# Kernel tuning notes

Hardware: AMD Instinct MI355X
Metric: run time of the kernel (lower is better)

The kernel has to match this reference:

```python
import jax, jax.numpy as jnp
import numpy as np

LEAK = 0.01  # torch LeakyReLU default negative_slope

def lrelu(x):
    return jnp.where(x >= 0, x, LEAK * x)

def edge_conv(x, src, dst, ea, W1, b1, W2, b2):
    # message: cat(x_i=target, x_j=source, edge_attr) -> Linear -> LeakyReLU -> Linear
    m = jnp.concatenate([x[dst], x[src], ea], axis=1)          # [E, 2F+Fe]
    h = lrelu(m @ W1 + b1) @ W2 + b2                            # [E, H]
    n = x.shape[0]
    agg = jnp.full((n, h.shape[1]), jnp.inf, h.dtype).at[dst].min(h)  # scatter-min at target
    return jnp.where(jnp.isfinite(agg), agg, jnp.zeros_like(agg))     # empty nodes -> 0


def setup_inputs() -> dict:
    key = jax.random.key(0)
    ks = jax.random.split(key, 20)
    B, N, E = 4, 20000, 640000
    NF, AD, EF, H = 2, 1, 1, 8
    inp = {
        "node_features": jax.random.randint(ks[0], (B, N, NF), 0, 10, dtype=jnp.int32),
        "actions": jax.random.normal(ks[1], (B, N), dtype=jnp.float32),
        "edge_index": jax.random.randint(ks[2], (B, 2, E), 0, N, dtype=jnp.int64),
        "edge_features": jax.random.normal(ks[3], (B, E, EF), dtype=jnp.float32),
    }
    d0 = NF + AD  # 3
    def lin(k, fin, fout):
        s = 1.0 / np.sqrt(fin)
        k1, k2 = jax.random.split(k)
        return (jax.random.uniform(k1, (fin, fout), jnp.float32, -s, s),
                jax.random.uniform(k2, (fout,), jnp.float32, -s, s))
    inp["c1_W1"], inp["c1_b1"] = lin(ks[4], 2 * d0 + EF, H)
    inp["c1_W2"], inp["c1_b2"] = lin(ks[5], H, H)
    inp["c2_W1"], inp["c2_b1"] = lin(ks[6], 2 * H + 1, H)
    inp["c2_W2"], inp["c2_b2"] = lin(ks[7], H, H)
    inp["c3_W1"], inp["c3_b1"] = lin(ks[8], 2 * H + 1, H)
    inp["c3_W2"], inp["c3_b2"] = lin(ks[9], H, H)
    inp["lin_W"], inp["lin_b"] = lin(ks[10], d0 + H, 1)
    return inp


def reference(node_features, actions, edge_index, edge_features,
              c1_W1, c1_b1, c1_W2, c1_b2,
              c2_W1, c2_b1, c2_W2, c2_b2,
              c3_W1, c3_b1, c3_W2, c3_b2,
              lin_W, lin_b):
    # x = int(node_features) concat actions  -> float
    x0 = jnp.concatenate([node_features.astype(jnp.int32).astype(jnp.float32),
                          actions[..., None]], axis=-1)  # [B,N,3]

    def per_graph(x0g, eig, eag):
        src, dst = eig[0], eig[1]  # flow source_to_target: x_j=src, x_i=dst
        h = lrelu(edge_conv(x0g, src, dst, eag, c1_W1, c1_b1, c1_W2, c1_b2))
        h = lrelu(edge_conv(h, src, dst, eag, c2_W1, c2_b1, c2_W2, c2_b2))
        h = lrelu(edge_conv(h, src, dst, eag, c3_W1, c3_b1, c3_W2, c3_b2))
        xc = jnp.concatenate([x0g, h], axis=1)  # [N, 3+8]
        return jnp.sum(xc, axis=0)              # sum-pool over nodes

    pooled = jax.vmap(per_graph)(x0, edge_index, edge_features)  # [B, 11]
    return pooled @ lin_W + lin_b  # [B, 1]
```

## Files before the change

kernel.cpp:

```cpp
#include <hip/hip_runtime.h>

#define LEAK 0.01f
#define BS 128
#define PCHUNK 4096
#define PT 256
#define CT 512
#define MAXNB 256
#define CPGMAX 256

__device__ __forceinline__ float lrelu(float v) {
    return v >= 0.f ? v : LEAK * v;
}

__device__ __forceinline__ unsigned int fmin_encode(float x) {
    unsigned int u = __float_as_uint(x);
    return (u & 0x80000000u) ? ~u : (u | 0x80000000u);
}
__device__ __forceinline__ float fmin_decode(unsigned int k) {
    unsigned int u = (k & 0x80000000u) ? (k ^ 0x80000000u) : ~k;
    return __uint_as_float(u);
}

__device__ __forceinline__ void block_add(float c, float* dst) {
    __shared__ float wsum[8];
#pragma unroll
    for (int off = 32; off > 0; off >>= 1) c += __shfl_down(c, off, 64);
    int lane = threadIdx.x & 63;
    int wave = threadIdx.x >> 6;
    if (lane == 0) wsum[wave] = c;
    __syncthreads();
    if (threadIdx.x == 0) {
        float s = 0.f;
        int nw = blockDim.x >> 6;
        for (int w = 0; w < nw; ++w) s += wsum[w];
        atomicAdd(dst, s);
    }
}

__global__ __launch_bounds__(256) void init_pre1_kernel(
    const int* __restrict__ nf, const float* __restrict__ act,
    const float* __restrict__ W1, const float* __restrict__ b1,
    const float* __restrict__ lw, const float* __restrict__ lb,
    float* __restrict__ a1, float* __restrict__ a2,
    float* __restrict__ out, int N) {
    int b = blockIdx.y;
    int n = blockIdx.x * 256 + threadIdx.x;
    float c = 0.f;
    if (n < N) {
        size_t i = (size_t)b * N + n;
        float x0 = (float)nf[i * 2 + 0];
        float x1 = (float)nf[i * 2 + 1];
        float x2 = act[i];
        float v1[8], v2[8];
#pragma unroll
        for (int j = 0; j < 8; ++j) {
            v1[j] = b1[j] + x0 * W1[0 * 8 + j] + x1 * W1[1 * 8 + j] + x2 * W1[2 * 8 + j];
            v2[j] =         x0 * W1[3 * 8 + j] + x1 * W1[4 * 8 + j] + x2 * W1[5 * 8 + j];
        }
        float4* o1 = (float4*)(a1 + i * 8);
        float4* o2 = (float4*)(a2 + i * 8);
        o1[0] = make_float4(v1[0], v1[1], v1[2], v1[3]);
        o1[1] = make_float4(v1[4], v1[5], v1[6], v1[7]);
        o2[0] = make_float4(v2[0], v2[1], v2[2], v2[3]);
        o2[1] = make_float4(v2[4], v2[5], v2[6], v2[7]);
        c = x0 * lw[0] + x1 * lw[1] + x2 * lw[2];
        if (n == 0) c += lb[0];
    }
    block_add(c, &out[b]);
}

__global__ __launch_bounds__(PT) void part_kernel(
    const int* __restrict__ ei, const float* __restrict__ ea,
    int2* __restrict__ pairs, int* __restrict__ ofs,
    int E, int NB, int CPG) {
    __shared__ int lc[MAXNB];
    __shared__ int lofs[MAXNB + 1];
    __shared__ int ts[PT];
    int b = blockIdx.y;
    int c = blockIdx.x;
    int t = threadIdx.x;
    for (int i = t; i < NB; i += PT) lc[i] = 0;
    __syncthreads();

    int e0 = c * PCHUNK;
    int end = min(e0 + PCHUNK, E);
    const int* srow = ei + (size_t)b * 2 * E;
    const int* drow = srow + E;

    int pk[PCHUNK / PT];
#pragma unroll
    for (int j = 0; j < PCHUNK / PT; ++j) {
        int e = e0 + j * PT + t;
        int p = -1;
        if (e < end) {
            int d = drow[e];
            int bin = d >> 7;
            int r = atomicAdd(&lc[bin], 1);
            p = bin | ((d & 127) << 10) | (r << 17);
        }
        pk[j] = p;
    }
    __syncthreads();

    int v = (t < NB) ? lc[t] : 0;
    ts[t] = v;
    __syncthreads();
    int incl = v;
    for (int off = 1; off < PT; off <<= 1) {
        int add = (t >= off) ? ts[t - off] : 0;
        __syncthreads();
        incl += add;
        ts[t] = incl;
        __syncthreads();
    }
    if (t < NB) lofs[t] = incl - v;
    if (t == PT - 1) lofs[NB] = incl;
    __syncthreads();

    int* og = ofs + ((size_t)b * CPG + c) * (NB + 1);
    for (int i = t; i <= NB; i += PT) {
        int w = lofs[i];
        og[i] = w;
        if (i < NB) lc[i] = w;
    }
    __syncthreads();

    size_t pbase = (size_t)b * E + e0;
#pragma unroll
    for (int j = 0; j < PCHUNK / PT; ++j) {
        int e = e0 + j * PT + t;
        if (e < end) {
            int p = pk[j];
            int bin = p & 1023;
            int dl = (p >> 10) & 127;
            int r = p >> 17;
            int pos = lc[bin] + r;
            pairs[pbase + pos] =
                make_int2(srow[e] | (dl << 16), __float_as_int(ea[(size_t)b * E + e]));
        }
    }
}


__device__ __forceinline__ void conv_edge_body(
    const float* __restrict__ a2g, const float* we, const float* bb,
    const float* __restrict__ W2, int2 p,
    const float* __restrict__ a1s, unsigned int* __restrict__ acc) {
    int srcn = p.x & 0xFFFF;
    int dl = (p.x >> 16) & 127;
    float eav = __int_as_float(p.y);
    const float4* q = (const float4*)(a2g + (size_t)srcn * 8);
    float4 lo = q[0], hi = q[1];
    float h1[8];
    h1[0] = a1s[dl * 9 + 0] + lo.x; h1[1] = a1s[dl * 9 + 1] + lo.y;
    h1[2] = a1s[dl * 9 + 2] + lo.z; h1[3] = a1s[dl * 9 + 3] + lo.w;
    h1[4] = a1s[dl * 9 + 4] + hi.x; h1[5] = a1s[dl * 9 + 5] + hi.y;
    h1[6] = a1s[dl * 9 + 6] + hi.z; h1[7] = a1s[dl * 9 + 7] + hi.w;
#pragma unroll
    for (int j = 0; j < 8; ++j) {
        h1[j] = fmaf(eav, we[j], h1[j]);
        h1[j] = lrelu(h1[j]);
    }
    float h2[8];
#pragma unroll
    for (int j = 0; j < 8; ++j) h2[j] = bb[j];
#pragma unroll
    for (int kk = 0; kk < 8; ++kk) {
        float hk = h1[kk];
#pragma unroll
        for (int j = 0; j < 8; ++j) h2[j] = fmaf(hk, W2[kk * 8 + j], h2[j]);
    }
#pragma unroll
    for (int j = 0; j < 8; ++j)
        atomicMin(&acc[dl * 9 + j], fmin_encode(h2[j]));
}

__device__ __forceinline__ void conv_edges_runs(
    const float* __restrict__ a2g, const float* we, const float* bb,
    const float* __restrict__ W2, const int2* __restrict__ pairsg,
    const int* __restrict__ ofsg, int bin, int NB, int CPG,
    const float* __restrict__ a1s, unsigned int* __restrict__ acc,
    int* __restrict__ rs, int* __restrict__ re) {
    int t = threadIdx.x;
    for (int c = t; c < CPG; c += CT) {
        const int* o = ofsg + (size_t)c * (NB + 1) + bin;
        rs[c] = o[0];
        re[c] = o[1];
    }
    __syncthreads();
    int sw = t >> 5;
    int sub = t & 31;
    const int nsw = CT >> 5;
    for (int c = sw; c < CPG; c += nsw) {
        int cb = c * PCHUNK;
        int k1 = cb + re[c];
        for (int k = cb + rs[c] + sub; k < k1; k += 32)
            conv_edge_body(a2g, we, bb, W2, pairsg[k], a1s, acc);
    }
}

__global__ __launch_bounds__(CT) void conv_mid_kernel(
    const float* __restrict__ a1, const float* __restrict__ a2,
    const float* __restrict__ w1e, const float* __restrict__ W2,
    const float* __restrict__ b2,
    const float* __restrict__ nW1, const float* __restrict__ nb1,
    const int* __restrict__ ofs, const int2* __restrict__ pairs,
    float* __restrict__ na1, float* __restrict__ na2,
    int N, int NB, int CPG, int E) {
    __shared__ float a1s[BS * 9];
    __shared__ unsigned int acc[BS * 9];
    __shared__ int rs[CPGMAX];
    __shared__ int re[CPGMAX];
    int b = blockIdx.y;
    int bin = blockIdx.x;
    int n0 = bin << 7;
    int nCnt = min(BS, N - n0);
    int t = threadIdx.x;
    size_t gn0 = ((size_t)b * N + n0) * 8;

    for (int i = t; i < nCnt * 8; i += CT)
        a1s[(i >> 3) * 9 + (i & 7)] = a1[gn0 + i];
    for (int i = t; i < BS * 9; i += CT) acc[i] = 0xFFFFFFFFu;
    float we[8], bb[8];
#pragma unroll
    for (int j = 0; j < 8; ++j) { we[j] = w1e[j]; bb[j] = b2[j]; }
    __syncthreads();

    conv_edges_runs(a2 + (size_t)b * N * 8, we, bb, W2,
                    pairs + (size_t)b * E, ofs + (size_t)b * CPG * (NB + 1),
                    bin, NB, CPG, a1s, acc, rs, re);
    __syncthreads();

    for (int i = t; i < nCnt * 8; i += CT) {
        float v = fmin_decode(acc[(i >> 3) * 9 + (i & 7)]);
        unsigned int u = __float_as_uint(v);
        if ((u & 0x7F800000u) == 0x7F800000u) v = 0.f;
        a1s[(i >> 3) * 9 + (i & 7)] = lrelu(v);
    }
    __syncthreads();

    int node = t >> 1, half = t & 1;
    if (node < nCnt) {
        float h[8];
#pragma unroll
        for (int j = 0; j < 8; ++j) h[j] = a1s[node * 9 + j];
        float v[8];
#pragma unroll
        for (int j = 0; j < 8; ++j) v[j] = half ? 0.f : nb1[j];
        const float* Wbase = nW1 + (half ? 64 : 0);
#pragma unroll
        for (int k = 0; k < 8; ++k) {
            float hk = h[k];
#pragma unroll
            for (int j = 0; j < 8; ++j) v[j] = fmaf(hk, Wbase[k * 8 + j], v[j]);
        }
        float* dst = (half ? na2 : na1) + gn0 + (size_t)node * 8;
        float4* o = (float4*)dst;
        o[0] = make_float4(v[0], v[1], v[2], v[3]);
        o[1] = make_float4(v[4], v[5], v[6], v[7]);
    }
}

__global__ __launch_bounds__(CT) void conv_final_kernel(
    const float* __restrict__ a1, const float* __restrict__ a2,
    const float* __restrict__ w1e, const float* __restrict__ W2,
    const float* __restrict__ b2, const float* __restrict__ lw,
    const int* __restrict__ ofs, const int2* __restrict__ pairs,
    float* __restrict__ out, int N, int NB, int CPG, int E) {
    __shared__ float a1s[BS * 9];
    __shared__ unsigned int acc[BS * 9];
    __shared__ int rs[CPGMAX];
    __shared__ int re[CPGMAX];
    int b = blockIdx.y;
    int bin = blockIdx.x;
    int n0 = bin << 7;
    int nCnt = min(BS, N - n0);
    int t = threadIdx.x;
    size_t gn0 = ((size_t)b * N + n0) * 8;

    for (int i = t; i < nCnt * 8; i += CT)
        a1s[(i >> 3) * 9 + (i & 7)] = a1[gn0 + i];
    for (int i = t; i < BS * 9; i += CT) acc[i] = 0xFFFFFFFFu;
    float we[8], bb[8];
#pragma unroll
    for (int j = 0; j < 8; ++j) { we[j] = w1e[j]; bb[j] = b2[j]; }
    __syncthreads();

    conv_edges_runs(a2 + (size_t)b * N * 8, we, bb, W2,
                    pairs + (size_t)b * E, ofs + (size_t)b * CPG * (NB + 1),
                    bin, NB, CPG, a1s, acc, rs, re);
    __syncthreads();

    float c = 0.f;
    if (t < nCnt) {
#pragma unroll
        for (int j = 0; j < 8; ++j) {
            float v = fmin_decode(acc[t * 9 + j]);
            unsigned int u = __float_as_uint(v);
            if ((u & 0x7F800000u) == 0x7F800000u) v = 0.f;
            c = fmaf(lrelu(v), lw[3 + j], c);
        }
    }
    __syncthreads();
    block_add(c, &out[b]);
}


__global__ __launch_bounds__(256) void node_init_kernel(
    const int* __restrict__ nf, const float* __restrict__ act,
    float* __restrict__ x0, int BN) {
    int tid = blockIdx.x * blockDim.x + threadIdx.x;
    if (tid >= BN) return;
    x0[tid * 3 + 0] = (float)nf[tid * 2 + 0];
    x0[tid * 3 + 1] = (float)nf[tid * 2 + 1];
    x0[tid * 3 + 2] = act[tid];
}

template <int D>
__global__ __launch_bounds__(256) void edge_conv_kernel(
    const float* __restrict__ x, const int* __restrict__ ei,
    const float* __restrict__ ea,
    const float* __restrict__ W1, const float* __restrict__ b1,
    const float* __restrict__ W2, const float* __restrict__ b2,
    unsigned int* __restrict__ agg, int E, int N, int B) {
    int tid = blockIdx.x * blockDim.x + threadIdx.x;
    if (tid >= B * E) return;
    int b = tid / E;
    int e = tid - b * E;
    const int* eb = ei + (size_t)b * 2 * E;
    int s = eb[e];
    int d = eb[E + e];
    const float* xi = x + ((size_t)b * N + d) * D;
    const float* xj = x + ((size_t)b * N + s) * D;
    constexpr int M = 2 * D + 1;
    float m[M];
#pragma unroll
    for (int k = 0; k < D; ++k) { m[k] = xi[k]; m[D + k] = xj[k]; }
    m[2 * D] = ea[(size_t)b * E + e];
    float h1[8];
#pragma unroll
    for (int j = 0; j < 8; ++j) h1[j] = b1[j];
#pragma unroll
    for (int k = 0; k < M; ++k) {
        float mk = m[k];
#pragma unroll
        for (int j = 0; j < 8; ++j) h1[j] = fmaf(mk, W1[k * 8 + j], h1[j]);
    }
#pragma unroll
    for (int j = 0; j < 8; ++j) h1[j] = lrelu(h1[j]);
    float h2[8];
#pragma unroll
    for (int j = 0; j < 8; ++j) h2[j] = b2[j];
#pragma unroll
    for (int k = 0; k < 8; ++k) {
        float hk = h1[k];
#pragma unroll
        for (int j = 0; j < 8; ++j) h2[j] = fmaf(hk, W2[k * 8 + j], h2[j]);
    }
    unsigned int* ag = agg + ((size_t)b * N + d) * 8;
#pragma unroll
    for (int j = 0; j < 8; ++j) atomicMin(&ag[j], fmin_encode(h2[j]));
}

__global__ __launch_bounds__(256) void finalize_kernel(
    unsigned int* __restrict__ agg, int total) {
    int tid = blockIdx.x * blockDim.x + threadIdx.x;
    if (tid >= total) return;
    float v = fmin_decode(agg[tid]);
    unsigned int u = __float_as_uint(v);
    if ((u & 0x7F800000u) == 0x7F800000u) v = 0.f;
    ((float*)agg)[tid] = lrelu(v);
}

__global__ __launch_bounds__(256) void pool_kernel(
    const float* __restrict__ x0, const float* __restrict__ h,
    const float* __restrict__ lw, const float* __restrict__ lb,
    float* __restrict__ out, int N) {
    int b = blockIdx.y;
    int n = blockIdx.x * blockDim.x + threadIdx.x;
    float c = 0.f;
    if (n < N) {
        const float* x = x0 + ((size_t)b * N + n) * 3;
        const float* hh = h + ((size_t)b * N + n) * 8;
        c = x[0] * lw[0] + x[1] * lw[1] + x[2] * lw[2];
#pragma unroll
        for (int k = 0; k < 8; ++k) c = fmaf(hh[k], lw[3 + k], c);
        if (n == 0) c += lb[0];
    }
    block_add(c, &out[b]);
}


static inline size_t align256(size_t x) { return (x + 255) & ~(size_t)255; }

extern "C" void kernel_launch(void* const* d_in, const int* in_sizes, int n_in,
                              void* d_out, int out_size, void* d_ws, size_t ws_size,
                              hipStream_t stream) {
    const int B = 4;
    const int N = in_sizes[1] / B;
    const int E = in_sizes[2] / (2 * B);

    const int*   nf  = (const int*)d_in[0];
    const float* act = (const float*)d_in[1];
    const int*   ei  = (const int*)d_in[2];
    const float* ea  = (const float*)d_in[3];
    const float* c1_W1 = (const float*)d_in[4];
    const float* c1_b1 = (const float*)d_in[5];
    const float* c1_W2 = (const float*)d_in[6];
    const float* c1_b2 = (const float*)d_in[7];
    const float* c2_W1 = (const float*)d_in[8];
    const float* c2_b1 = (const float*)d_in[9];
    const float* c2_W2 = (const float*)d_in[10];
    const float* c2_b2 = (const float*)d_in[11];
    const float* c3_W1 = (const float*)d_in[12];
    const float* c3_b1 = (const float*)d_in[13];
    const float* c3_W2 = (const float*)d_in[14];
    const float* c3_b2 = (const float*)d_in[15];
    const float* lw    = (const float*)d_in[16];
    const float* lb    = (const float*)d_in[17];
    float* out = (float*)d_out;

    const int BN = B * N;
    const int BE = B * E;
    const int NB = (N + BS - 1) / BS;
    const int CPG = (E + PCHUNK - 1) / PCHUNK;

    char* ws = (char*)d_ws;
    size_t off = 0;
    float* a1A  = (float*)(ws + off);  off += align256((size_t)BN * 8 * 4);
    float* a2A  = (float*)(ws + off);  off += align256((size_t)BN * 8 * 4);
    float* a1B  = (float*)(ws + off);  off += align256((size_t)BN * 8 * 4);
    float* a2B  = (float*)(ws + off);  off += align256((size_t)BN * 8 * 4);
    int* ofs    = (int*)(ws + off);    off += align256((size_t)B * CPG * (NB + 1) * 4);
    int2* pairs = (int2*)(ws + off);   off += align256((size_t)BE * 8);
    float* x0   = (float*)(ws + off);  off += align256((size_t)BN * 3 * 4);
    const bool useFast = (off <= ws_size) && (NB <= MAXNB) && (CPG <= CPGMAX) &&
                         (N <= 32768);

    hipMemsetAsync(out, 0, (size_t)B * sizeof(float), stream);

    if (useFast) {
        dim3 pgrid(CPG, B);
        dim3 igrid((N + 255) / 256, B);
        dim3 cgrid(NB, B);

        init_pre1_kernel<<<igrid, 256, 0, stream>>>(nf, act, c1_W1, c1_b1,
                                                    lw, lb, a1A, a2A, out, N);
        part_kernel<<<pgrid, PT, 0, stream>>>(ei, ea, pairs, ofs, E, NB, CPG);

        conv_mid_kernel<<<cgrid, CT, 0, stream>>>(
            a1A, a2A, c1_W1 + 6 * 8, c1_W2, c1_b2, c2_W1, c2_b1,
            ofs, pairs, a1B, a2B, N, NB, CPG, E);
        conv_mid_kernel<<<cgrid, CT, 0, stream>>>(
            a1B, a2B, c2_W1 + 16 * 8, c2_W2, c2_b2, c3_W1, c3_b1,
            ofs, pairs, a1A, a2A, N, NB, CPG, E);
        conv_final_kernel<<<cgrid, CT, 0, stream>>>(
            a1A, a2A, c3_W1 + 16 * 8, c3_W2, c3_b2, lw,
            ofs, pairs, out, N, NB, CPG, E);
    } else {
        const int egrid = (BE + 255) / 256;
        const int aggTotal = BN * 8;
        const int agrid = (aggTotal + 255) / 256;
        const size_t aggBytes = (size_t)aggTotal * 4;
        unsigned int* uA = (unsigned int*)a1A;
        unsigned int* uB = (unsigned int*)a1B;

        node_init_kernel<<<(BN + 255) / 256, 256, 0, stream>>>(nf, act, x0, BN);

        hipMemsetAsync(uA, 0xFF, aggBytes, stream);
        edge_conv_kernel<3><<<egrid, 256, 0, stream>>>(
            x0, ei, ea, c1_W1, c1_b1, c1_W2, c1_b2, uA, E, N, B);
        finalize_kernel<<<agrid, 256, 0, stream>>>(uA, aggTotal);

        hipMemsetAsync(uB, 0xFF, aggBytes, stream);
        edge_conv_kernel<8><<<egrid, 256, 0, stream>>>(
            (const float*)uA, ei, ea, c2_W1, c2_b1, c2_W2, c2_b2, uB, E, N, B);
        finalize_kernel<<<agrid, 256, 0, stream>>>(uB, aggTotal);

        hipMemsetAsync(uA, 0xFF, aggBytes, stream);
        edge_conv_kernel<8><<<egrid, 256, 0, stream>>>(
            (const float*)uB, ei, ea, c3_W1, c3_b1, c3_W2, c3_b2, uA, E, N, B);
        finalize_kernel<<<agrid, 256, 0, stream>>>(uA, aggTotal);

        dim3 plgrid((N + 255) / 256, B);
        pool_kernel<<<plgrid, 256, 0, stream>>>(x0, (const float*)uA, lw, lb, out, N);
    }
}
```

Baseline: 221.3 us.

## Transpose offset table, prefetch next chunk's first pair, widen partition block

The per-chunk bin offset table is stored bin-major instead of chunk-major, so each conv block reads its start and end offsets for all chunks with coalesced loads. The edge loop in the conv kernels now software-prefetches the first pair of the next chunk before processing the current one, to hide gather latency. The partition kernel block size is doubled from 256 to 512 threads, which changes its scan and scatter loop shapes. The partition kernel now writes offsets with a strided pattern, and the larger block may reduce its occupancy.

Result: no change. 222.1 us (+0.4%).

```diff
diff --git a/kernel.cpp b/kernel.cpp
--- a/kernel.cpp
+++ b/kernel.cpp
@@ -3,7 +3,7 @@
 #define LEAK 0.01f
 #define BS 128
 #define PCHUNK 4096
-#define PT 256
+#define PT 512
 #define CT 512
 #define MAXNB 256
 #define CPGMAX 256
@@ -117,10 +117,9 @@
     if (t == PT - 1) lofs[NB] = incl;
     __syncthreads();
 
-    int* og = ofs + ((size_t)b * CPG + c) * (NB + 1);
     for (int i = t; i <= NB; i += PT) {
         int w = lofs[i];
-        og[i] = w;
+        ofs[((size_t)b * (NB + 1) + i) * CPG + c] = w;
         if (i < NB) lc[i] = w;
     }
     __syncthreads();
@@ -178,24 +177,42 @@
 __device__ __forceinline__ void conv_edges_runs(
     const float* __restrict__ a2g, const float* we, const float* bb,
     const float* __restrict__ W2, const int2* __restrict__ pairsg,
-    const int* __restrict__ ofsg, int bin, int NB, int CPG,
+    const int* __restrict__ ofb, int CPG,
     const float* __restrict__ a1s, unsigned int* __restrict__ acc,
     int* __restrict__ rs, int* __restrict__ re) {
     int t = threadIdx.x;
     for (int c = t; c < CPG; c += CT) {
-        const int* o = ofsg + (size_t)c * (NB + 1) + bin;
-        rs[c] = o[0];
-        re[c] = o[1];
-    }
-    __syncthreads();
-    int sw = t >> 5;
-    int sub = t & 31;
+        rs[c] = ofb[c];
+        re[c] = ofb[CPG + c];
+    }
+    __syncthreads();
+    int sw = t >> 5, sub = t & 31;
     const int nsw = CT >> 5;
-    for (int c = sw; c < CPG; c += nsw) {
+    int c = sw;
+    int2 pcur = make_int2(0, 0);
+    int kcur = 0, k1cur = 0;
+    if (c < CPG) {
         int cb = c * PCHUNK;
-        int k1 = cb + re[c];
-        for (int k = cb + rs[c] + sub; k < k1; k += 32)
-            conv_edge_body(a2g, we, bb, W2, pairsg[k], a1s, acc);
+        kcur = cb + rs[c] + sub;
+        k1cur = cb + re[c];
+        if (kcur < k1cur) pcur = pairsg[kcur];
+    }
+    while (c < CPG) {
+        int cn = c + nsw;
+        int2 pnext = make_int2(0, 0);
+        int knext = 0, k1next = 0;
+        if (cn < CPG) {
+            int cb = cn * PCHUNK;
+            knext = cb + rs[cn] + sub;
+            k1next = cb + re[cn];
+            if (knext < k1next) pnext = pairsg[knext];
+        }
+        if (kcur < k1cur) {
+            conv_edge_body(a2g, we, bb, W2, pcur, a1s, acc);
+            for (int k = kcur + 32; k < k1cur; k += 32)
+                conv_edge_body(a2g, we, bb, W2, pairsg[k], a1s, acc);
+        }
+        c = cn; kcur = knext; k1cur = k1next; pcur = pnext;
     }
 }
 
@@ -227,8 +244,9 @@
     __syncthreads();
 
     conv_edges_runs(a2 + (size_t)b * N * 8, we, bb, W2,
-                    pairs + (size_t)b * E, ofs + (size_t)b * CPG * (NB + 1),
-                    bin, NB, CPG, a1s, acc, rs, re);
+                    pairs + (size_t)b * E,
+                    ofs + ((size_t)b * (NB + 1) + bin) * CPG,
+                    CPG, a1s, acc, rs, re);
     __syncthreads();
 
     for (int i = t; i < nCnt * 8; i += CT) {
@@ -287,8 +305,9 @@
     __syncthreads();
 
     conv_edges_runs(a2 + (size_t)b * N * 8, we, bb, W2,
-                    pairs + (size_t)b * E, ofs + (size_t)b * CPG * (NB + 1),
-                    bin, NB, CPG, a1s, acc, rs, re);
+                    pairs + (size_t)b * E,
+                    ofs + ((size_t)b * (NB + 1) + bin) * CPG,
+                    CPG, a1s, acc, rs, re);
     __syncthreads();
 
     float c = 0.f;
@@ -431,7 +450,7 @@
     float* a2A  = (float*)(ws + off);  off += align256((size_t)BN * 8 * 4);
     float* a1B  = (float*)(ws + off);  off += align256((size_t)BN * 8 * 4);
     float* a2B  = (float*)(ws + off);  off += align256((size_t)BN * 8 * 4);
-    int* ofs    = (int*)(ws + off);    off += align256((size_t)B * CPG * (NB + 1) * 4);
+    int* ofs    = (int*)(ws + off);    off += align256((size_t)B * (NB + 1) * CPG * 4);
     int2* pairs = (int2*)(ws + off);   off += align256((size_t)BE * 8);
     float* x0   = (float*)(ws + off);  off += align256((size_t)BN * 3 * 4);
     const bool useFast = (off <= ws_size) && (NB <= MAXNB) && (CPG <= CPGMAX) &&
```
